# Performance work log

Measured on AMD Instinct MI355X. Metric: run time of the kernel, lower is better.

## Reference

```python
import jax, jax.numpy as jnp
import numpy as np

E = 262144
D = 128          # node/edge latent dim
H = 512          # MLP hidden dim
IN = 3 * D       # concat of x_i, x_j, edge_attr
LN_EPS = 1e-5


def setup_inputs() -> dict:
    key = jax.random.key(0)
    ks = jax.random.split(key, 9)
    s1 = 1.0 / np.sqrt(IN)
    s2 = 1.0 / np.sqrt(H)
    return {
        "x_i": jax.random.normal(ks[0], (E, D), dtype=jnp.float32),
        "x_j": jax.random.normal(ks[1], (E, D), dtype=jnp.float32),
        "edge_attr": jax.random.normal(ks[2], (E, D), dtype=jnp.float32),
        "W1": jax.random.uniform(ks[3], (IN, H), jnp.float32, -s1, s1),
        "b1": jax.random.uniform(ks[4], (H,), jnp.float32, -s1, s1),
        "W2": jax.random.uniform(ks[5], (H, D), jnp.float32, -s2, s2),
        "b2": jax.random.uniform(ks[6], (D,), jnp.float32, -s2, s2),
        "gamma": jnp.ones((D,), dtype=jnp.float32),
        "beta": jnp.zeros((D,), dtype=jnp.float32),
    }


def reference(x_i, x_j, edge_attr, W1, b1, W2, b2, gamma, beta):
    # concat -> Linear -> SiLU -> Linear -> LayerNorm -> +edge_attr (residual)
    h = jnp.concatenate([x_i, x_j, edge_attr], axis=-1)        # [E, 3D]
    h = jax.nn.silu(h @ W1 + b1)                                # [E, H]
    h = h @ W2 + b2                                             # [E, D]
    mu = jnp.mean(h, axis=-1, keepdims=True)
    var = jnp.mean(jnp.square(h - mu), axis=-1, keepdims=True)
    h = (h - mu) * jax.lax.rsqrt(var + LN_EPS) * gamma + beta   # LayerNorm
    return h + edge_attr
```

## Files before the change

### kernel.cpp

```cpp
#include <hip/hip_runtime.h>
#include <hip/hip_bf16.h>

typedef __bf16 bf16;
typedef __attribute__((ext_vector_type(8))) __bf16 bf16x8;
typedef __attribute__((ext_vector_type(4))) float f32x4;

#define E_EDGES 262144
#define MT 128

__global__ void transpose_w(const float* __restrict__ W1, const float* __restrict__ W2,
                            bf16* __restrict__ W1t, bf16* __restrict__ W2t)
{
  int tid = blockIdx.x * 256 + threadIdx.x;
  if (tid < 512 * 384) {
    int n = tid / 384;
    int k = tid - n * 384;
    W1t[tid] = (bf16)W1[k * 512 + n];
  }
  if (tid < 128 * 512) {
    int n = tid >> 9;
    int k = tid & 511;
    W2t[tid] = (bf16)W2[k * 128 + n];
  }
}

__device__ __forceinline__ bf16x8 cvt8v(f32x4 a, f32x4 b) {
  bf16x8 r;
  r[0] = (bf16)a[0]; r[1] = (bf16)a[1]; r[2] = (bf16)a[2]; r[3] = (bf16)a[3];
  r[4] = (bf16)b[0]; r[5] = (bf16)b[1]; r[6] = (bf16)b[2]; r[7] = (bf16)b[3];
  return r;
}

__device__ __forceinline__ void glds16(const void* g, void* l) {
  __builtin_amdgcn_global_load_lds(
      (const __attribute__((address_space(1))) void*)g,
      (__attribute__((address_space(3))) void*)l,
      16, 0, 0);
}

__global__ __launch_bounds__(512, 4)
void fused_edge_mlp(const float* __restrict__ x_i,
                    const float* __restrict__ x_j,
                    const float* __restrict__ ea,
                    const bf16* __restrict__ W1t,
                    const float* __restrict__ b1,
                    const bf16* __restrict__ W2t,
                    const float* __restrict__ b2,
                    const float* __restrict__ gmm,
                    const float* __restrict__ bta,
                    float* __restrict__ out)
{
  __shared__ bf16 As[2][128 * 32];
  __shared__ bf16 Bs[2][128 * 32];
  __shared__ bf16 H1s[128 * 136];

  const int t    = threadIdx.x;
  const int w    = t >> 6;
  const int lane = t & 63;
  const int l15  = lane & 15;
  const int q    = lane >> 4;
  const int srow = t >> 2;
  const int sc   = t & 3;
  const int scf  = sc << 3;
  const int swz  = (sc ^ ((srow >> 1) & 3)) << 3;
  const int rsw  = (l15 >> 1) & 3;
  const int wm   = w >> 2;
  const int wn   = w & 3;
  const long m0  = (long)blockIdx.x * MT;
  const int wb   = (t & ~63) << 3;

  const f32x4 fzero = {0.f, 0.f, 0.f, 0.f};

  float b1r[8];
  #pragma unroll
  for (int j = 0; j < 8; ++j)
    b1r[j] = b1[(j >> 1) * 128 + 32 * wn + 16 * (j & 1) + l15];

  f32x4 acc2[8];
  #pragma unroll
  for (int i = 0; i < 8; ++i) acc2[i] = fzero;

  {
    const float* pA = x_i + (m0 + srow) * 128 + scf;
    f32x4 a0 = *(const f32x4*)pA;
    f32x4 a1 = *(const f32x4*)(pA + 4);
    glds16(W1t + (long)srow * 384 + swz, &Bs[0][wb]);
    *(bf16x8*)&As[0][srow * 32 + swz] = cvt8v(a0, a1);
    __syncthreads();
  }

  int p = 0;
  for (int nc = 0; nc < 4; ++nc) {
    f32x4 acc1[8];
    #pragma unroll
    for (int i = 0; i < 8; ++i) acc1[i] = fzero;

    for (int kk = 0; kk < 12; ++kk) {
      f32x4 a0, a1;
      if (kk < 11) {
        const int k1 = kk + 1;
        const float* sA = (k1 < 4) ? x_i : (k1 < 8) ? x_j : ea;
        const float* pA = sA + (m0 + srow) * 128 + ((k1 & 3) << 5) + scf;
        a0 = *(const f32x4*)pA;
        a1 = *(const f32x4*)(pA + 4);
        glds16(W1t + (long)(nc * 128 + srow) * 384 + (k1 << 5) + swz, &Bs[p ^ 1][wb]);
      } else {
        glds16(W2t + (long)srow * 512 + (nc << 7) + swz, &As[p ^ 1][wb]);
      }

      bf16x8 af[4], bfr[2];
      #pragma unroll
      for (int mi = 0; mi < 4; ++mi)
        af[mi] = *(const bf16x8*)&As[p][(64 * wm + 16 * mi + l15) * 32 + ((q ^ rsw) << 3)];
      #pragma unroll
      for (int ni = 0; ni < 2; ++ni)
        bfr[ni] = *(const bf16x8*)&Bs[p][(32 * wn + 16 * ni + l15) * 32 + ((q ^ rsw) << 3)];
      #pragma unroll
      for (int mi = 0; mi < 4; ++mi)
        #pragma unroll
        for (int ni = 0; ni < 2; ++ni)
          acc1[mi * 2 + ni] = __builtin_amdgcn_mfma_f32_16x16x32_bf16(
              af[mi], bfr[ni], acc1[mi * 2 + ni], 0, 0, 0);

      if (kk < 11) {
        *(bf16x8*)&As[p ^ 1][srow * 32 + swz] = cvt8v(a0, a1);
      } else {
        #pragma unroll
        for (int mi = 0; mi < 4; ++mi)
          #pragma unroll
          for (int ni = 0; ni < 2; ++ni)
            #pragma unroll
            for (int i = 0; i < 4; ++i) {
              float s = acc1[mi * 2 + ni][i] + b1r[(nc << 1) + ni];
              float h = s / (1.f + __expf(-s));
              H1s[(64 * wm + 16 * mi + 4 * q + i) * 136 + 32 * wn + 16 * ni + l15] = (bf16)h;
            }
      }
      __syncthreads();
      p ^= 1;
    }

    for (int s4 = 0; s4 < 4; ++s4) {
      f32x4 a0, a1;
      bool stA = false;
      if (s4 < 3) {
        glds16(W2t + (long)srow * 512 + (nc << 7) + ((s4 + 1) << 5) + swz, &As[p ^ 1][wb]);
      } else if (nc < 3) {
        glds16(W1t + (long)((nc + 1) * 128 + srow) * 384 + swz, &Bs[p ^ 1][wb]);
        const float* pA = x_i + (m0 + srow) * 128 + scf;
        a0 = *(const f32x4*)pA;
        a1 = *(const f32x4*)(pA + 4);
        stA = true;
      }

      bf16x8 a2 = *(const bf16x8*)&H1s[(16 * w + l15) * 136 + (s4 << 5) + (q << 3)];
      #pragma unroll
      for (int ni = 0; ni < 8; ++ni) {
        bf16x8 b2f = *(const bf16x8*)&As[p][(16 * ni + l15) * 32 + ((q ^ rsw) << 3)];
        acc2[ni] = __builtin_amdgcn_mfma_f32_16x16x32_bf16(a2, b2f, acc2[ni], 0, 0, 0);
      }

      if (stA)
        *(bf16x8*)&As[p ^ 1][srow * 32 + swz] = cvt8v(a0, a1);
      __syncthreads();
      p ^= 1;
    }
  }

  float b2v[8], gv[8], bv[8];
  #pragma unroll
  for (int ni = 0; ni < 8; ++ni) {
    int n = 16 * ni + l15;
    b2v[ni] = b2[n];
    gv[ni]  = gmm[n];
    bv[ni]  = bta[n];
  }
  #pragma unroll
  for (int ni = 0; ni < 8; ++ni)
    #pragma unroll
    for (int i = 0; i < 4; ++i)
      acc2[ni][i] += b2v[ni];

  #pragma unroll
  for (int i = 0; i < 4; ++i) {
    float s = 0.f, s2 = 0.f;
    #pragma unroll
    for (int ni = 0; ni < 8; ++ni) {
      float v = acc2[ni][i];
      s += v;
      s2 += v * v;
    }
    #pragma unroll
    for (int off = 1; off <= 8; off <<= 1) {
      s  += __shfl_xor(s,  off, 64);
      s2 += __shfl_xor(s2, off, 64);
    }
    float mu   = s * (1.f / 128.f);
    float var  = fmaxf(s2 * (1.f / 128.f) - mu * mu, 0.f);
    float rstd = rsqrtf(var + 1e-5f);
    long  mg   = m0 + 16 * w + 4 * q + i;
    #pragma unroll
    for (int ni = 0; ni < 8; ++ni) {
      int n = 16 * ni + l15;
      float o = (acc2[ni][i] - mu) * rstd * gv[ni] + bv[ni] + ea[mg * 128 + n];
      out[mg * 128 + n] = o;
    }
  }
}

extern "C" void kernel_launch(void* const* d_in, const int* in_sizes, int n_in,
                              void* d_out, int out_size, void* d_ws, size_t ws_size,
                              hipStream_t stream)
{
  const float* x_i = (const float*)d_in[0];
  const float* x_j = (const float*)d_in[1];
  const float* ea  = (const float*)d_in[2];
  const float* W1  = (const float*)d_in[3];
  const float* b1  = (const float*)d_in[4];
  const float* W2  = (const float*)d_in[5];
  const float* b2  = (const float*)d_in[6];
  const float* gm  = (const float*)d_in[7];
  const float* bt  = (const float*)d_in[8];
  float* outp = (float*)d_out;
  bf16* W1t = (bf16*)d_ws;
  bf16* W2t = W1t + 512 * 384;

  hipLaunchKernelGGL(transpose_w, dim3(768), dim3(256), 0, stream, W1, W2, W1t, W2t);
  hipLaunchKernelGGL(fused_edge_mlp, dim3(E_EDGES / MT), dim3(512), 0, stream,
                     x_i, x_j, ea, W1t, b1, W2t, b2, gm, bt, outp);
}
```

Before: 636.2 us.

## Triple-buffer weight tiles with two-ahead prefetch and manual waitcnt barriers

Merges the GEMM1 and GEMM2 stage loops into one fully unrolled 16-step loop per hidden chunk. Weight tiles are now triple-buffered and prefetched two steps ahead, with activations held in registers two steps ahead. __syncthreads is replaced by explicit vmcnt/lgkmcnt waits plus s_barrier, and MFMA sections are wrapped with s_setprio, so global loads have more time in flight before they are consumed. The cost is more LDS and registers and fragile hand-written wait counts, which risk races if a count is wrong.

```diff
diff --git a/kernel.cpp b/kernel.cpp
--- a/kernel.cpp
+++ b/kernel.cpp
@@ -7,6 +7,11 @@
 
 #define E_EDGES 262144
 #define MT 128
+
+#define VMW(n)  asm volatile("s_waitcnt vmcnt(" #n ")" ::: "memory")
+#define LGKM0   asm volatile("s_waitcnt lgkmcnt(0)" ::: "memory")
+#define FENCE   asm volatile("" ::: "memory")
+#define BAR     __builtin_amdgcn_s_barrier()
 
 __global__ void transpose_w(const float* __restrict__ W1, const float* __restrict__ W2,
                             bf16* __restrict__ W1t, bf16* __restrict__ W2t)
@@ -51,7 +56,7 @@
                     float* __restrict__ out)
 {
   __shared__ bf16 As[2][128 * 32];
-  __shared__ bf16 Bs[2][128 * 32];
+  __shared__ bf16 Bs[3][128 * 32];
   __shared__ bf16 H1s[128 * 136];
 
   const int t    = threadIdx.x;
@@ -80,51 +85,87 @@
   #pragma unroll
   for (int i = 0; i < 8; ++i) acc2[i] = fzero;
 
+  f32x4 ar[2][2];
+
+  glds16(W1t + (long)srow * 384 + swz, &Bs[0][wb]);
+  FENCE;
   {
-    const float* pA = x_i + (m0 + srow) * 128 + scf;
-    f32x4 a0 = *(const f32x4*)pA;
-    f32x4 a1 = *(const f32x4*)(pA + 4);
-    glds16(W1t + (long)srow * 384 + swz, &Bs[0][wb]);
-    *(bf16x8*)&As[0][srow * 32 + swz] = cvt8v(a0, a1);
-    __syncthreads();
-  }
-
-  int p = 0;
+    const float* p = x_i + (m0 + srow) * 128 + scf;
+    ar[0][0] = *(const f32x4*)p;  ar[0][1] = *(const f32x4*)(p + 4);
+  }
+  FENCE;
+  glds16(W1t + (long)srow * 384 + 32 + swz, &Bs[1][wb]);
+  FENCE;
+  {
+    const float* p = x_i + (m0 + srow) * 128 + 32 + scf;
+    ar[1][0] = *(const f32x4*)p;  ar[1][1] = *(const f32x4*)(p + 4);
+  }
+  FENCE;
+  *(bf16x8*)&As[0][srow * 32 + swz] = cvt8v(ar[0][0], ar[0][1]);
+  LGKM0;
+  BAR;
+
   for (int nc = 0; nc < 4; ++nc) {
     f32x4 acc1[8];
     #pragma unroll
     for (int i = 0; i < 8; ++i) acc1[i] = fzero;
 
-    for (int kk = 0; kk < 12; ++kk) {
-      f32x4 a0, a1;
-      if (kk < 11) {
-        const int k1 = kk + 1;
-        const float* sA = (k1 < 4) ? x_i : (k1 < 8) ? x_j : ea;
-        const float* pA = sA + (m0 + srow) * 128 + ((k1 & 3) << 5) + scf;
-        a0 = *(const f32x4*)pA;
-        a1 = *(const f32x4*)(pA + 4);
-        glds16(W1t + (long)(nc * 128 + srow) * 384 + (k1 << 5) + swz, &Bs[p ^ 1][wb]);
+    #pragma unroll
+    for (int j = 0; j < 16; ++j) {
+      const int buf  = (nc + j) % 3;
+      const int tbuf = (nc + j + 2) % 3;
+
+      {
+        const int tt = j + 2;
+        if (tt < 12) {
+          glds16(W1t + (long)(nc * 128 + srow) * 384 + (tt << 5) + swz, &Bs[tbuf][wb]);
+          FENCE;
+          const float* s = (tt < 4) ? x_i : (tt < 8) ? x_j : ea;
+          const float* p = s + (m0 + srow) * 128 + ((tt & 3) << 5) + scf;
+          ar[j & 1][0] = *(const f32x4*)p;  ar[j & 1][1] = *(const f32x4*)(p + 4);
+          FENCE;
+        } else if (tt < 16) {
+          glds16(W2t + (long)srow * 512 + (nc << 7) + ((tt - 12) << 5) + swz, &Bs[tbuf][wb]);
+          FENCE;
+        } else if (nc < 3) {
+          glds16(W1t + (long)((nc + 1) * 128 + srow) * 384 + ((tt - 16) << 5) + swz,
+                 &Bs[tbuf][wb]);
+          FENCE;
+          const float* p = x_i + (m0 + srow) * 128 + ((tt - 16) << 5) + scf;
+          ar[j & 1][0] = *(const f32x4*)p;  ar[j & 1][1] = *(const f32x4*)(p + 4);
+          FENCE;
+        }
+      }
+
+      if (j < 12) {
+        bf16x8 af[4], bfr[2];
+        #pragma unroll
+        for (int mi = 0; mi < 4; ++mi)
+          af[mi] = *(const bf16x8*)&As[j & 1][(64 * wm + 16 * mi + l15) * 32 + ((q ^ rsw) << 3)];
+        #pragma unroll
+        for (int ni = 0; ni < 2; ++ni)
+          bfr[ni] = *(const bf16x8*)&Bs[buf][(32 * wn + 16 * ni + l15) * 32 + ((q ^ rsw) << 3)];
+        __builtin_amdgcn_s_setprio(1);
+        #pragma unroll
+        for (int mi = 0; mi < 4; ++mi)
+          #pragma unroll
+          for (int ni = 0; ni < 2; ++ni)
+            acc1[mi * 2 + ni] = __builtin_amdgcn_mfma_f32_16x16x32_bf16(
+                af[mi], bfr[ni], acc1[mi * 2 + ni], 0, 0, 0);
+        __builtin_amdgcn_s_setprio(0);
       } else {
-        glds16(W2t + (long)srow * 512 + (nc << 7) + swz, &As[p ^ 1][wb]);
-      }
-
-      bf16x8 af[4], bfr[2];
-      #pragma unroll
-      for (int mi = 0; mi < 4; ++mi)
-        af[mi] = *(const bf16x8*)&As[p][(64 * wm + 16 * mi + l15) * 32 + ((q ^ rsw) << 3)];
-      #pragma unroll
-      for (int ni = 0; ni < 2; ++ni)
-        bfr[ni] = *(const bf16x8*)&Bs[p][(32 * wn + 16 * ni + l15) * 32 + ((q ^ rsw) << 3)];
-      #pragma unroll
-      for (int mi = 0; mi < 4; ++mi)
-        #pragma unroll
-        for (int ni = 0; ni < 2; ++ni)
-          acc1[mi * 2 + ni] = __builtin_amdgcn_mfma_f32_16x16x32_bf16(
-              af[mi], bfr[ni], acc1[mi * 2 + ni], 0, 0, 0);
-
-      if (kk < 11) {
-        *(bf16x8*)&As[p ^ 1][srow * 32 + swz] = cvt8v(a0, a1);
-      } else {
+        const int s4 = j - 12;
+        bf16x8 a2 = *(const bf16x8*)&H1s[(16 * w + l15) * 136 + (s4 << 5) + (q << 3)];
+        __builtin_amdgcn_s_setprio(1);
+        #pragma unroll
+        for (int ni = 0; ni < 8; ++ni) {
+          bf16x8 b2f = *(const bf16x8*)&Bs[buf][(16 * ni + l15) * 32 + ((q ^ rsw) << 3)];
+          acc2[ni] = __builtin_amdgcn_mfma_f32_16x16x32_bf16(a2, b2f, acc2[ni], 0, 0, 0);
+        }
+        __builtin_amdgcn_s_setprio(0);
+      }
+
+      if (j == 11) {
         #pragma unroll
         for (int mi = 0; mi < 4; ++mi)
           #pragma unroll
@@ -136,34 +177,23 @@
               H1s[(64 * wm + 16 * mi + 4 * q + i) * 136 + 32 * wn + 16 * ni + l15] = (bf16)h;
             }
       }
-      __syncthreads();
-      p ^= 1;
-    }
-
-    for (int s4 = 0; s4 < 4; ++s4) {
-      f32x4 a0, a1;
-      bool stA = false;
-      if (s4 < 3) {
-        glds16(W2t + (long)srow * 512 + (nc << 7) + ((s4 + 1) << 5) + swz, &As[p ^ 1][wb]);
-      } else if (nc < 3) {
-        glds16(W1t + (long)((nc + 1) * 128 + srow) * 384 + swz, &Bs[p ^ 1][wb]);
-        const float* pA = x_i + (m0 + srow) * 128 + scf;
-        a0 = *(const f32x4*)pA;
-        a1 = *(const f32x4*)(pA + 4);
-        stA = true;
-      }
-
-      bf16x8 a2 = *(const bf16x8*)&H1s[(16 * w + l15) * 136 + (s4 << 5) + (q << 3)];
-      #pragma unroll
-      for (int ni = 0; ni < 8; ++ni) {
-        bf16x8 b2f = *(const bf16x8*)&As[p][(16 * ni + l15) * 32 + ((q ^ rsw) << 3)];
-        acc2[ni] = __builtin_amdgcn_mfma_f32_16x16x32_bf16(a2, b2f, acc2[ni], 0, 0, 0);
-      }
-
-      if (stA)
-        *(bf16x8*)&As[p ^ 1][srow * 32 + swz] = cvt8v(a0, a1);
-      __syncthreads();
-      p ^= 1;
+
+      if (j <= 10 || (j == 15 && nc < 3)) {
+        FENCE;
+        *(bf16x8*)&As[(j + 1) & 1][srow * 32 + swz] =
+            cvt8v(ar[(j + 1) & 1][0], ar[(j + 1) & 1][1]);
+      }
+
+      if (j == 11) VMW(1);
+      if (j == 12) VMW(1);
+      if (j == 13) VMW(1);
+      if (j == 14) {
+        if (nc < 3) VMW(3);
+        else        VMW(0);
+      }
+
+      LGKM0;
+      BAR;
     }
   }
 
```

New measurement: 845.5 us. 32.9% more time.
